# Optimization experiments

Measured on AMD Instinct MI355X. Metric: run time of the kernel, lower is better.

## Reference

```python
import jax, jax.numpy as jnp
import numpy as np

D = 6          # atom_dims, fixed by GroupNorm(2, D) and reshape(-1, 6)
K = 16         # neighbors
N_LAYERS = 3
C_IN = 2 * D + 1  # 13
EPS = 1e-5
SLOPE = 0.2


def _lrelu(x):
    return jnp.where(x >= 0, x, SLOPE * x)


def _group_norm(x, w, b):
    # x: [M, D], 2 groups of D//2 channels, affine per channel
    m = x.shape[0]
    xg = x.reshape(m, 2, D // 2)
    mu = xg.mean(-1, keepdims=True)
    var = xg.var(-1, keepdims=True)
    xn = ((xg - mu) * jax.lax.rsqrt(var + EPS)).reshape(m, D)
    return xn * w + b


def setup_inputs() -> dict:
    key = jax.random.key(0)
    ks = jax.random.split(key, 8)
    B, N = 4, 100000
    dist = jax.random.uniform(ks[0], (B, N, K, 1), dtype=jnp.float32)
    atomtypes = jax.random.uniform(ks[1], (B, N, K, D), dtype=jnp.float32)
    s1 = 1.0 / np.sqrt(C_IN)
    W1 = jax.random.uniform(ks[2], (N_LAYERS, C_IN, C_IN), jnp.float32, -s1, s1)
    b1 = jax.random.uniform(ks[3], (N_LAYERS, C_IN), jnp.float32, -s1, s1)
    W2 = jax.random.uniform(ks[4], (N_LAYERS, C_IN, D), jnp.float32, -s1, s1)
    b2 = jax.random.uniform(ks[5], (N_LAYERS, D), jnp.float32, -s1, s1)
    gw = jnp.ones((N_LAYERS, D), jnp.float32)
    gb = jnp.zeros((N_LAYERS, D), jnp.float32)
    return {"dist": dist, "atomtypes": atomtypes, "W1": W1, "b1": b1,
            "W2": W2, "b2": b2, "gw": gw, "gb": gb}


def reference(dist, atomtypes, W1, b1, W2, b2, gw, gb):
    B, N, k, d = atomtypes.shape
    point_emb = jnp.ones((B, N, d), dtype=atomtypes.dtype)
    for i in range(N_LAYERS):
        # [B,N,k,2D+1]: broadcast point emb to neighbors, concat atom feats + dist
        feat = jnp.concatenate(
            [jnp.broadcast_to(point_emb[:, :, None, :], (B, N, k, d)),
             atomtypes, dist], axis=-1)
        h = _lrelu(jnp.einsum('bnkc,cd->bnkd', feat, W1[i]) + b1[i])
        msg = (jnp.einsum('bnkc,cd->bnkd', h, W2[i]) + b2[i]).sum(-2)  # [B,N,D]
        upd = _lrelu(_group_norm(msg.reshape(-1, d), gw[i], gb[i])).reshape(B, N, d)
        point_emb = point_emb + upd
    return point_emb
```

## Files before the change

kernel.cpp:

```cpp
#include <hip/hip_runtime.h>


constexpr int DD  = 6;
constexpr int KK  = 16;
constexpr int CIN = 13;
constexpr float EPSV  = 1e-5f;
constexpr float SLOPE = 0.2f;

__global__ __launch_bounds__(256) void atom_mp(
    const float* __restrict__ dist,
    const float* __restrict__ at,
    const float* __restrict__ W1,
    const float* __restrict__ b1,
    const float* __restrict__ W2,
    const float* __restrict__ b2,
    const float* __restrict__ gw,
    const float* __restrict__ gb,
    float* __restrict__ out,
    int P)
{
    int p = blockIdx.x * blockDim.x + threadIdx.x;
    if (p >= P) return;

    float a[KK * DD];
    float dd[KK];

    const float4* ap4 = reinterpret_cast<const float4*>(at + (long)p * (KK * DD));
    #pragma unroll
    for (int i = 0; i < (KK * DD) / 4; ++i) {
        float4 q = ap4[i];
        a[4 * i + 0] = q.x; a[4 * i + 1] = q.y;
        a[4 * i + 2] = q.z; a[4 * i + 3] = q.w;
    }
    const float4* dp4 = reinterpret_cast<const float4*>(dist + (long)p * KK);
    #pragma unroll
    for (int i = 0; i < KK / 4; ++i) {
        float4 q = dp4[i];
        dd[4 * i + 0] = q.x; dd[4 * i + 1] = q.y;
        dd[4 * i + 2] = q.z; dd[4 * i + 3] = q.w;
    }

    float pe[DD] = {1.f, 1.f, 1.f, 1.f, 1.f, 1.f};

    #pragma unroll 1
    for (int L = 0; L < 3; ++L) {
        const float* w1  = W1 + L * CIN * CIN;
        const float* w2  = W2 + L * CIN * DD;
        const float* bb1 = b1 + L * CIN;
        const float* bb2 = b2 + L * DD;
        const float* gwp = gw + L * DD;
        const float* gbp = gb + L * DD;

        float base[CIN];
        #pragma unroll
        for (int d = 0; d < CIN; ++d) {
            float s = bb1[d];
            #pragma unroll
            for (int c = 0; c < DD; ++c)
                s = fmaf(pe[c], w1[c * CIN + d], s);
            base[d] = s;
        }

        float hsum[CIN];
        #pragma unroll
        for (int d = 0; d < CIN; ++d) hsum[d] = 0.f;

        #pragma unroll
        for (int k = 0; k < KK; ++k) {
            float f[7] = {a[6 * k + 0], a[6 * k + 1], a[6 * k + 2],
                          a[6 * k + 3], a[6 * k + 4], a[6 * k + 5], dd[k]};
            #pragma unroll
            for (int d = 0; d < CIN; ++d) {
                float acc = base[d];
                #pragma unroll
                for (int j = 0; j < 7; ++j)
                    acc = fmaf(f[j], w1[(6 + j) * CIN + d], acc);
                hsum[d] += fmaxf(acc, SLOPE * acc);
            }
        }

        float msg[DD];
        #pragma unroll
        for (int d = 0; d < DD; ++d) {
            float m = 16.f * bb2[d];
            #pragma unroll
            for (int c = 0; c < CIN; ++c)
                m = fmaf(hsum[c], w2[c * DD + d], m);
            msg[d] = m;
        }

        #pragma unroll
        for (int g = 0; g < 2; ++g) {
            float m0 = msg[3 * g], m1 = msg[3 * g + 1], m2 = msg[3 * g + 2];
            float mu = (m0 + m1 + m2) * (1.f / 3.f);
            float d0 = m0 - mu, d1 = m1 - mu, d2 = m2 - mu;
            float var = (d0 * d0 + d1 * d1 + d2 * d2) * (1.f / 3.f);
            float rs = rsqrtf(var + EPSV);
            float dv[3] = {d0, d1, d2};
            #pragma unroll
            for (int c = 0; c < 3; ++c) {
                int ch = 3 * g + c;
                float xn = dv[c] * rs * gwp[ch] + gbp[ch];
                pe[ch] += fmaxf(xn, SLOPE * xn);
            }
        }
    }

    float2* op = reinterpret_cast<float2*>(out + (long)p * DD);
    op[0] = make_float2(pe[0], pe[1]);
    op[1] = make_float2(pe[2], pe[3]);
    op[2] = make_float2(pe[4], pe[5]);
}

extern "C" void kernel_launch(void* const* d_in, const int* in_sizes, int n_in,
                              void* d_out, int out_size, void* d_ws, size_t ws_size,
                              hipStream_t stream) {
    const float* dist = (const float*)d_in[0];
    const float* at   = (const float*)d_in[1];
    const float* W1   = (const float*)d_in[2];
    const float* b1   = (const float*)d_in[3];
    const float* W2   = (const float*)d_in[4];
    const float* b2   = (const float*)d_in[5];
    const float* gw   = (const float*)d_in[6];
    const float* gb   = (const float*)d_in[7];
    float* out = (float*)d_out;

    int P = in_sizes[0] / KK;
    int threads = 256;
    int blocks = (P + threads - 1) / threads;
    atom_mp<<<blocks, threads, 0, stream>>>(dist, at, W1, b1, W2, b2, gw, gb, out, P);
}
```

Baseline: 282.9 us.

## Split each point's neighbors across two lanes and combine with shuffle

Each point is now handled by two adjacent threads, each loading and processing 8 of the 16 neighbors, so per-thread register use drops and thread count doubles. Partial hidden sums are combined with a cross-lane xor shuffle, and both lanes then redundantly compute the small message, group norm and update. The loop order is changed to iterate output channel outermost with 8 independent accumulators. Leaky ReLU is rewritten as 0.6x+0.4|x|, folded into FMAs. The cost is duplicated per-point tail work on both lanes and a rounding change in the activation.

New measurement: 272.7 us. -3.6%, faster.

```diff
diff --git a/kernel.cpp b/kernel.cpp
--- a/kernel.cpp
+++ b/kernel.cpp
@@ -4,8 +4,7 @@
 constexpr int DD  = 6;
 constexpr int KK  = 16;
 constexpr int CIN = 13;
-constexpr float EPSV  = 1e-5f;
-constexpr float SLOPE = 0.2f;
+constexpr float EPSV = 1e-5f;
 
 __global__ __launch_bounds__(256) void atom_mp(
     const float* __restrict__ dist,
@@ -19,25 +18,29 @@
     float* __restrict__ out,
     int P)
 {
-    int p = blockIdx.x * blockDim.x + threadIdx.x;
+    int t = blockIdx.x * blockDim.x + threadIdx.x;
+    int p = t >> 1;
+    int h = t & 1;
     if (p >= P) return;
 
-    float a[KK * DD];
-    float dd[KK];
+    float a[8 * DD];
+    float dq[8];
 
-    const float4* ap4 = reinterpret_cast<const float4*>(at + (long)p * (KK * DD));
+    const float4* ap4 = reinterpret_cast<const float4*>(
+        at + (long)p * (KK * DD) + h * (8 * DD));
     #pragma unroll
-    for (int i = 0; i < (KK * DD) / 4; ++i) {
+    for (int i = 0; i < 12; ++i) {
         float4 q = ap4[i];
         a[4 * i + 0] = q.x; a[4 * i + 1] = q.y;
         a[4 * i + 2] = q.z; a[4 * i + 3] = q.w;
     }
-    const float4* dp4 = reinterpret_cast<const float4*>(dist + (long)p * KK);
+    const float4* dp4 = reinterpret_cast<const float4*>(
+        dist + (long)p * KK + h * 8);
     #pragma unroll
-    for (int i = 0; i < KK / 4; ++i) {
+    for (int i = 0; i < 2; ++i) {
         float4 q = dp4[i];
-        dd[4 * i + 0] = q.x; dd[4 * i + 1] = q.y;
-        dd[4 * i + 2] = q.z; dd[4 * i + 3] = q.w;
+        dq[4 * i + 0] = q.x; dq[4 * i + 1] = q.y;
+        dq[4 * i + 2] = q.z; dq[4 * i + 3] = q.w;
     }
 
     float pe[DD] = {1.f, 1.f, 1.f, 1.f, 1.f, 1.f};
@@ -51,33 +54,41 @@
         const float* gwp = gw + L * DD;
         const float* gbp = gb + L * DD;
 
-        float base[CIN];
+        float hsum[CIN];
+
         #pragma unroll
         for (int d = 0; d < CIN; ++d) {
             float s = bb1[d];
             #pragma unroll
             for (int c = 0; c < DD; ++c)
                 s = fmaf(pe[c], w1[c * CIN + d], s);
-            base[d] = s;
+
+            float w0 = w1[6 * CIN + d];
+            float acc[8];
+            #pragma unroll
+            for (int k = 0; k < 8; ++k)
+                acc[k] = fmaf(a[6 * k + 0], w0, s);
+            #pragma unroll
+            for (int j = 1; j < 7; ++j) {
+                float w = w1[(6 + j) * CIN + d];
+                #pragma unroll
+                for (int k = 0; k < 8; ++k) {
+                    float fv = (j < 6) ? a[6 * k + j] : dq[k];
+                    acc[k] = fmaf(fv, w, acc[k]);
+                }
+            }
+            float hs = 0.f;
+            #pragma unroll
+            for (int k = 0; k < 8; ++k) {
+                hs = fmaf(0.6f, acc[k], hs);
+                hs = fmaf(0.4f, __builtin_fabsf(acc[k]), hs);
+            }
+            hsum[d] = hs;
         }
 
-        float hsum[CIN];
         #pragma unroll
-        for (int d = 0; d < CIN; ++d) hsum[d] = 0.f;
-
-        #pragma unroll
-        for (int k = 0; k < KK; ++k) {
-            float f[7] = {a[6 * k + 0], a[6 * k + 1], a[6 * k + 2],
-                          a[6 * k + 3], a[6 * k + 4], a[6 * k + 5], dd[k]};
-            #pragma unroll
-            for (int d = 0; d < CIN; ++d) {
-                float acc = base[d];
-                #pragma unroll
-                for (int j = 0; j < 7; ++j)
-                    acc = fmaf(f[j], w1[(6 + j) * CIN + d], acc);
-                hsum[d] += fmaxf(acc, SLOPE * acc);
-            }
-        }
+        for (int d = 0; d < CIN; ++d)
+            hsum[d] += __shfl_xor(hsum[d], 1, 64);
 
         float msg[DD];
         #pragma unroll
@@ -100,16 +111,20 @@
             #pragma unroll
             for (int c = 0; c < 3; ++c) {
                 int ch = 3 * g + c;
-                float xn = dv[c] * rs * gwp[ch] + gbp[ch];
-                pe[ch] += fmaxf(xn, SLOPE * xn);
+                float xn = fmaf(dv[c] * rs, gwp[ch], gbp[ch]);
+                pe[ch] = fmaf(0.6f, xn, pe[ch]);
+                pe[ch] = fmaf(0.4f, __builtin_fabsf(xn), pe[ch]);
             }
         }
     }
 
-    float2* op = reinterpret_cast<float2*>(out + (long)p * DD);
-    op[0] = make_float2(pe[0], pe[1]);
-    op[1] = make_float2(pe[2], pe[3]);
-    op[2] = make_float2(pe[4], pe[5]);
+    float* op = out + (long)p * DD;
+    if (h == 0) {
+        *reinterpret_cast<float2*>(op)     = make_float2(pe[0], pe[1]);
+        *reinterpret_cast<float2*>(op + 2) = make_float2(pe[2], pe[3]);
+    } else {
+        *reinterpret_cast<float2*>(op + 4) = make_float2(pe[4], pe[5]);
+    }
 }
 
 extern "C" void kernel_launch(void* const* d_in, const int* in_sizes, int n_in,
@@ -126,7 +141,8 @@
     float* out = (float*)d_out;
 
     int P = in_sizes[0] / KK;
+    long threads_total = 2L * P;
     int threads = 256;
-    int blocks = (P + threads - 1) / threads;
+    int blocks = (int)((threads_total + threads - 1) / threads);
     atom_mp<<<blocks, threads, 0, stream>>>(dist, at, W1, b1, W2, b2, gw, gb, out, P);
 }
```
